# Kernel optimization log

Hardware: AMD Instinct MI355X
Metric: run time of the kernel (lower is better)

Reference implementation:

```python
import jax, jax.numpy as jnp
import numpy as np

N = 100000   # nodes
E = 1000000  # edges
G = 256      # graphs
IN, HID, OUT = 64, 64, 32


def _gcn_conv(x, W, b, src, dst, n_nodes):
    # PyG GCNConv with add_self_loops=True, symmetric normalization:
    # out = D^{-1/2} (A + I) D^{-1/2} X W + b
    h = x @ W  # [N, F]
    deg = jax.ops.segment_sum(jnp.ones_like(src, dtype=h.dtype), dst, num_segments=n_nodes) + 1.0
    dinv = jax.lax.rsqrt(deg)  # deg >= 1 due to self loops
    norm = dinv[src] * dinv[dst]  # [E]
    agg = jax.ops.segment_sum(h[src] * norm[:, None], dst, num_segments=n_nodes)
    agg = agg + h * (dinv * dinv)[:, None]  # self-loop contribution
    return agg + b


def setup_inputs() -> dict:
    key = jax.random.key(0)
    ks = jax.random.split(key, 12)
    x = jax.random.normal(ks[0], (N, IN), dtype=jnp.float32)
    edge_index = jax.random.randint(ks[1], (2, E), 0, N, dtype=jnp.int64)
    batch = jnp.sort(jax.random.randint(ks[2], (N,), 0, G, dtype=jnp.int64))

    def lin(k, fin, fout):
        s = 1.0 / np.sqrt(fin)
        kw, kb = jax.random.split(k)
        return (jax.random.uniform(kw, (fin, fout), minval=-s, maxval=s, dtype=jnp.float32),
                jax.random.uniform(kb, (fout,), minval=-s, maxval=s, dtype=jnp.float32))

    W1, b1 = lin(ks[3], IN, HID)
    W2, b2 = lin(ks[4], HID, HID)
    Wmu, bmu = lin(ks[5], HID, OUT)
    Wlv, blv = lin(ks[6], HID, OUT)
    Wd1, bd1 = lin(ks[7], OUT, HID)
    Wd2, bd2 = lin(ks[8], HID, IN)
    return {"x": x, "edge_index": edge_index, "batch": batch,
            "W1": W1, "b1": b1, "W2": W2, "b2": b2,
            "Wmu": Wmu, "bmu": bmu, "Wlv": Wlv, "blv": blv,
            "Wd1": Wd1, "bd1": bd1, "Wd2": Wd2, "bd2": bd2}


def reference(x, edge_index, batch, W1, b1, W2, b2, Wmu, bmu, Wlv, blv, Wd1, bd1, Wd2, bd2):
    src, dst = edge_index[0], edge_index[1]
    h = jax.nn.relu(_gcn_conv(x, W1, b1, src, dst, N))
    h = jax.nn.relu(_gcn_conv(h, W2, b2, src, dst, N))
    # global mean pool per graph
    sums = jax.ops.segment_sum(h, batch, num_segments=G)
    counts = jax.ops.segment_sum(jnp.ones((N,), dtype=h.dtype), batch, num_segments=G)
    pooled = sums / jnp.maximum(counts, 1.0)[:, None]  # [G, HID]
    mu = pooled @ Wmu + bmu
    logvar = pooled @ Wlv + blv
    eps = jax.random.normal(jax.random.key(42), mu.shape, dtype=mu.dtype)
    z = mu + eps * jnp.exp(0.5 * logvar)
    recon = jax.nn.relu(z @ Wd1 + bd1) @ Wd2 + bd2  # [G, IN]
    return recon, mu, logvar
```

## Files before the change

### kernel.cpp

```cpp
#include <hip/hip_runtime.h>
#include <hip/hip_bf16.h>

typedef __attribute__((ext_vector_type(8))) short bf16x8;
typedef __attribute__((ext_vector_type(4))) float f32x4;

__device__ inline unsigned short f2bf(float f) {
    unsigned u = __float_as_uint(f);
    unsigned r = u + 0x7fffu + ((u >> 16) & 1u);
    return (unsigned short)(r >> 16);
}
__device__ inline float bf2f(unsigned short s) {
    return __uint_as_float((unsigned)s << 16);
}


__device__ inline unsigned rotl32(unsigned x, unsigned r) {
    return (x << r) | (x >> (32 - r));
}

__device__ inline void threefry2x32_042(unsigned c0, unsigned c1,
                                        unsigned& o0, unsigned& o1) {
    const unsigned k0 = 0u, k1 = 42u;
    unsigned ks[3] = { k0, k1, k0 ^ k1 ^ 0x1BD11BDAu };
    unsigned x0 = c0 + ks[0];
    unsigned x1 = c1 + ks[1];
    const unsigned rotA[4] = {13u, 15u, 26u, 6u};
    const unsigned rotB[4] = {17u, 29u, 16u, 24u};

    #pragma unroll
    for (int i = 0; i < 5; ++i) {
        #pragma unroll
        for (int j = 0; j < 4; ++j) {
            unsigned r = (i & 1) ? rotB[j] : rotA[j];
            x0 += x1;
            x1 = rotl32(x1, r);
            x1 ^= x0;
        }
        x0 += ks[(i + 1) % 3];
        x1 += ks[(i + 2) % 3] + (unsigned)(i + 1);
    }
    o0 = x0; o1 = x1;
}

__device__ inline float erfinv_f32(float x) {
    float w = -log1pf(-x * x);
    float p;
    if (w < 5.0f) {
        w -= 2.5f;
        p = 2.81022636e-08f;
        p = fmaf(p, w, 3.43273939e-07f);
        p = fmaf(p, w, -3.5233877e-06f);
        p = fmaf(p, w, -4.39150654e-06f);
        p = fmaf(p, w, 0.00021858087f);
        p = fmaf(p, w, -0.00125372503f);
        p = fmaf(p, w, -0.00417768164f);
        p = fmaf(p, w, 0.246640727f);
        p = fmaf(p, w, 1.50140941f);
    } else {
        w = sqrtf(w) - 3.0f;
        p = -0.000200214257f;
        p = fmaf(p, w, 0.000100950558f);
        p = fmaf(p, w, 0.00134934322f);
        p = fmaf(p, w, -0.00367342844f);
        p = fmaf(p, w, 0.00573950773f);
        p = fmaf(p, w, -0.0076224613f);
        p = fmaf(p, w, 0.00943887047f);
        p = fmaf(p, w, 1.00167406f);
        p = fmaf(p, w, 2.83297682f);
    }
    return p * x;
}

__device__ inline float jax_normal_4232(unsigned idx) {
    unsigned o0, o1;
    threefry2x32_042(0u, idx, o0, o1);
    unsigned bits = o0 ^ o1;
    unsigned fb = (bits >> 9) | 0x3f800000u;
    float f = __uint_as_float(fb) - 1.0f;
    const float lo = -0.99999994f;
    float u = f * (1.0f - lo) + lo;
    u = fmaxf(u, lo);
    return 1.41421356f * erfinv_f32(u);
}


__device__ inline int idx_at(const void* p, long long i, int is64) {
    return is64 ? (int)((const long long*)p)[i] : ((const int*)p)[i];
}

#define NBK 256
#define CAP 4864

__global__ __launch_bounds__(256) void detect_idx64(const unsigned* __restrict__ raw,
                                                    int ne, int* flag,
                                                    int* __restrict__ bcnt,
                                                    int* __restrict__ gcur) {
    __shared__ int nz;
    if (threadIdx.x == 0) nz = 0;
    bcnt[threadIdx.x] = 0;
    gcur[threadIdx.x] = threadIdx.x * CAP;
    __syncthreads();
    int stride = ne / 2048;
    if (stride < 1) stride = 1;
    for (int k = threadIdx.x; k < 2048; k += 256) {
        long long j = (long long)k * stride;
        if (j < ne && raw[2 * j + 1] != 0u) nz = 1;
    }
    __syncthreads();
    if (threadIdx.x == 0) flag[0] = (nz == 0) ? 1 : 0;
}


#define CHUNK_MAX 4096

__global__ __launch_bounds__(256) void bucket_fill(const void* __restrict__ ei,
                                                   const int* __restrict__ flag,
                                                   int* __restrict__ gcur,
                                                   int* __restrict__ bcnt,
                                                   int2* __restrict__ pairs,
                                                   int ne, int npb, int chunk) {
    __shared__ int hist[NBK];
    __shared__ int basecur[NBK];
    __shared__ int sbuf[CHUNK_MAX];
    __shared__ int dbuf[CHUNK_MAX];
    int t = threadIdx.x;
    hist[t] = 0;
    __syncthreads();
    int is64 = flag[0];
    int c0 = blockIdx.x * chunk;
    int c1 = c0 + chunk; if (c1 > ne) c1 = ne;
    for (int i = c0 + t; i < c1; i += 256) {
        int s = idx_at(ei, i, is64);
        int d = idx_at(ei, (long long)ne + i, is64);
        sbuf[i - c0] = s;
        dbuf[i - c0] = d;
        atomicAdd(&hist[d / npb], 1);
    }
    __syncthreads();
    if (hist[t] > 0) {
        basecur[t] = atomicAdd(&gcur[t], hist[t]);
        atomicAdd(&bcnt[t], hist[t]);
    }
    __syncthreads();
    int nloc = c1 - c0;
    for (int li = t; li < nloc; li += 256) {
        int d = dbuf[li];
        int bb = d / npb;
        int slot = atomicAdd(&basecur[bb], 1);
        if (slot < (bb + 1) * CAP) pairs[slot] = make_int2(sbuf[li], d);
    }
}

#define NPB_MAX 512
__global__ __launch_bounds__(256) void csr_build(const int2* __restrict__ pairs,
                                                 const int* __restrict__ bcnt,
                                                 int* __restrict__ rowptr,
                                                 int* __restrict__ degarr,
                                                 float* __restrict__ dinv,
                                                 int* __restrict__ csr_src,
                                                 float* __restrict__ sums, int gtot,
                                                 int n, int npb) {
    __shared__ int cnt[NPB_MAX];
    __shared__ int cur[NPB_MAX];
    int b = blockIdx.x;
    int t = threadIdx.x;
    int gi = b * 256 + t;
    if (gi < gtot) sums[gi] = 0.0f;
    int bstart = b * npb;
    int bn = n - bstart; if (bn > npb) bn = npb;
    if (bn <= 0) return;
    int e0 = b * CAP;
    int count = bcnt[b]; if (count > CAP) count = CAP;
    int e1 = e0 + count;

    for (int i = t; i < bn; i += 256) cnt[i] = 0;
    __syncthreads();
    for (int i = e0 + t; i < e1; i += 256)
        atomicAdd(&cnt[pairs[i].y - bstart], 1);
    __syncthreads();

    if (t < 64) {
        int running = 0;
        for (int base2 = 0; base2 < bn; base2 += 64) {
            int idx2 = base2 + t;
            int v = (idx2 < bn) ? cnt[idx2] : 0;
            int orig = v;
            #pragma unroll
            for (int off = 1; off < 64; off <<= 1) {
                int tmp = __shfl_up(v, off);
                if (t >= off) v += tmp;
            }
            if (idx2 < bn) cur[idx2] = e0 + running + (v - orig);
            running += __shfl(v, 63);
        }
    }
    __syncthreads();

    for (int ln = t; ln < bn; ln += 256) {
        rowptr[bstart + ln] = cur[ln];
        degarr[bstart + ln] = cnt[ln];
        dinv[bstart + ln] = rsqrtf((float)cnt[ln] + 1.0f);
    }
    __syncthreads();

    for (int i = e0 + t; i < e1; i += 256) {
        int2 p = pairs[i];
        int slot = atomicAdd(&cur[p.y - bstart], 1);
        csr_src[slot] = p.x;
    }
}


__device__ inline void load_wfrags(const float* __restrict__ W,
                                   int cq, int cr, bf16x8 wf[2][4]) {
    #pragma unroll
    for (int ks = 0; ks < 2; ++ks)
        #pragma unroll
        for (int cb = 0; cb < 4; ++cb) {
            bf16x8 v;
            #pragma unroll
            for (int j = 0; j < 8; ++j) {
                int k = ks * 32 + cq * 8 + j;
                v[j] = (short)f2bf(W[k * 64 + cb * 16 + cr]);
            }
            wf[ks][cb] = v;
        }
}

__device__ inline void mfma_store(f32x4 acc[4], const float* __restrict__ dinv,
                                  unsigned short* __restrict__ Y,
                                  int rowbase, int cq, int cr, int nrows) {
    #pragma unroll
    for (int reg = 0; reg < 4; ++reg) {
        int r = rowbase + cq * 4 + reg;
        if (r < nrows) {
            float dv = dinv[r];
            #pragma unroll
            for (int cb = 0; cb < 4; ++cb)
                Y[(size_t)r * 64 + cb * 16 + cr] = f2bf(acc[cb][reg] * dv);
        }
    }
}

__global__ __launch_bounds__(256) void lin64_mfma_f32(const float* __restrict__ X,
                                                      const float* __restrict__ W,
                                                      const float* __restrict__ dinv,
                                                      unsigned short* __restrict__ Y,
                                                      int nrows) {
    int t = threadIdx.x;
    int lane = t & 63, wid = t >> 6;
    int cq = lane >> 4, cr = lane & 15;
    bf16x8 wf[2][4];
    load_wfrags(W, cq, cr, wf);
    int rowbase = (blockIdx.x * 4 + wid) * 16;
    if (rowbase >= nrows) return;
    int arow = rowbase + cr; if (arow >= nrows) arow = nrows - 1;
    const float* xr = X + (size_t)arow * 64;
    bf16x8 af[2];
    #pragma unroll
    for (int ks = 0; ks < 2; ++ks) {
        const float4* p = (const float4*)(xr + ks * 32 + cq * 8);
        float4 a = p[0], b = p[1];
        bf16x8 v;
        v[0] = (short)f2bf(a.x); v[1] = (short)f2bf(a.y);
        v[2] = (short)f2bf(a.z); v[3] = (short)f2bf(a.w);
        v[4] = (short)f2bf(b.x); v[5] = (short)f2bf(b.y);
        v[6] = (short)f2bf(b.z); v[7] = (short)f2bf(b.w);
        af[ks] = v;
    }
    f32x4 z = {0.0f, 0.0f, 0.0f, 0.0f};
    f32x4 acc[4] = {z, z, z, z};
    #pragma unroll
    for (int ks = 0; ks < 2; ++ks)
        #pragma unroll
        for (int cb = 0; cb < 4; ++cb)
            acc[cb] = __builtin_amdgcn_mfma_f32_16x16x32_bf16(af[ks], wf[ks][cb],
                                                              acc[cb], 0, 0, 0);
    mfma_store(acc, dinv, Y, rowbase, cq, cr, nrows);
}

__global__ __launch_bounds__(256) void lin64_mfma_bf16(const unsigned short* __restrict__ X,
                                                       const float* __restrict__ bin,
                                                       const float* __restrict__ W,
                                                       const float* __restrict__ dinv,
                                                       unsigned short* __restrict__ Y,
                                                       int nrows) {
    int t = threadIdx.x;
    int lane = t & 63, wid = t >> 6;
    int cq = lane >> 4, cr = lane & 15;
    bf16x8 wf[2][4];
    load_wfrags(W, cq, cr, wf);
    float bpre[2][8];
    #pragma unroll
    for (int ks = 0; ks < 2; ++ks)
        #pragma unroll
        for (int j = 0; j < 8; ++j)
            bpre[ks][j] = bin[ks * 32 + cq * 8 + j];
    int rowbase = (blockIdx.x * 4 + wid) * 16;
    if (rowbase >= nrows) return;
    int arow = rowbase + cr; if (arow >= nrows) arow = nrows - 1;
    const unsigned short* xr = X + (size_t)arow * 64;
    bf16x8 af[2];
    #pragma unroll
    for (int ks = 0; ks < 2; ++ks) {
        bf16x8 raw = *(const bf16x8*)(xr + ks * 32 + cq * 8);
        bf16x8 v;
        #pragma unroll
        for (int j = 0; j < 8; ++j) {
            float vv = bf2f((unsigned short)raw[j]) + bpre[ks][j];
            v[j] = (short)f2bf(fmaxf(vv, 0.0f));
        }
        af[ks] = v;
    }
    f32x4 z = {0.0f, 0.0f, 0.0f, 0.0f};
    f32x4 acc[4] = {z, z, z, z};
    #pragma unroll
    for (int ks = 0; ks < 2; ++ks)
        #pragma unroll
        for (int cb = 0; cb < 4; ++cb)
            acc[cb] = __builtin_amdgcn_mfma_f32_16x16x32_bf16(af[ks], wf[ks][cb],
                                                              acc[cb], 0, 0, 0);
    mfma_store(acc, dinv, Y, rowbase, cq, cr, nrows);
}


__global__ __launch_bounds__(256) void gcn_gather(const unsigned short* __restrict__ A,
                                                  const float* __restrict__ dinv,
                                                  const int* __restrict__ rowptr,
                                                  const int* __restrict__ degarr,
                                                  const int* __restrict__ csr_src,
                                                  unsigned short* __restrict__ B, int n) {
    int t = threadIdx.x;
    int node = blockIdx.x * 4 + (t >> 6);
    int c = t & 63;
    if (node >= n) return;
    float acc = bf2f(A[(size_t)node * 64 + c]);
    int beg = rowptr[node];
    int mt = degarr[node];
    for (int chunk = 0; chunk < mt; chunk += 64) {
        int m = mt - chunk; if (m > 64) m = 64;
        int sl = (c < m) ? csr_src[beg + chunk + c] : 0;
        for (int j0 = 0; j0 < m; j0 += 16) {
            int mm = m - j0; if (mm > 16) mm = 16;
            int sidx[16];
            #pragma unroll
            for (int j = 0; j < 16; ++j)
                sidx[j] = __shfl(sl, j < mm ? j0 + j : j0);
            float v[16];
            #pragma unroll
            for (int j = 0; j < 16; ++j)
                v[j] = bf2f(A[(size_t)sidx[j] * 64 + c]);
            #pragma unroll
            for (int j = 0; j < 16; ++j)
                v[j] = (j < mm) ? v[j] : 0.0f;
            float s01 = (v[0] + v[1]) + (v[2] + v[3]);
            float s23 = (v[4] + v[5]) + (v[6] + v[7]);
            float s45 = (v[8] + v[9]) + (v[10] + v[11]);
            float s67 = (v[12] + v[13]) + (v[14] + v[15]);
            acc += (s01 + s23) + (s45 + s67);
        }
    }
    B[(size_t)node * 64 + c] = f2bf(acc * dinv[node]);
}

#define POOL_NPW 32
__global__ __launch_bounds__(256) void pool_seg(const __hip_bfloat16* __restrict__ X,
                                                const float* __restrict__ b,
                                                const void* __restrict__ batch,
                                                const int* __restrict__ flag,
                                                float* __restrict__ sums,
                                                float* __restrict__ counts, int n) {
    int t = threadIdx.x;
    int c = t & 63;
    int wid = blockIdx.x * 4 + (t >> 6);
    int s0 = wid * POOL_NPW;
    if (s0 >= n) return;
    int s1 = s0 + POOL_NPW; if (s1 > n) s1 = n;
    int is64 = flag[0];
    float bc = b[c];
    float acc = 0.0f, cnt = 0.0f;
    int cur = idx_at(batch, s0, is64);
    int i = s0;
    for (; i + 2 <= s1; i += 2) {
        int g0 = idx_at(batch, i, is64);
        int g1 = idx_at(batch, i + 1, is64);
        float v0 = __bfloat162float(X[(size_t)i * 64 + c]);
        float v1 = __bfloat162float(X[(size_t)(i + 1) * 64 + c]);
        if (g0 != cur) {
            atomicAdd(&sums[(size_t)cur * 64 + c], acc);
            if (c == 0) atomicAdd(&counts[cur], cnt);
            acc = 0.0f; cnt = 0.0f; cur = g0;
        }
        acc += fmaxf(v0 + bc, 0.0f); cnt += 1.0f;
        if (g1 != cur) {
            atomicAdd(&sums[(size_t)cur * 64 + c], acc);
            if (c == 0) atomicAdd(&counts[cur], cnt);
            acc = 0.0f; cnt = 0.0f; cur = g1;
        }
        acc += fmaxf(v1 + bc, 0.0f); cnt += 1.0f;
    }
    if (i < s1) {
        int g0 = idx_at(batch, i, is64);
        float v0 = __bfloat162float(X[(size_t)i * 64 + c]);
        if (g0 != cur) {
            atomicAdd(&sums[(size_t)cur * 64 + c], acc);
            if (c == 0) atomicAdd(&counts[cur], cnt);
            acc = 0.0f; cnt = 0.0f; cur = g0;
        }
        acc += fmaxf(v0 + bc, 0.0f); cnt += 1.0f;
    }
    atomicAdd(&sums[(size_t)cur * 64 + c], acc);
    if (c == 0) atomicAdd(&counts[cur], cnt);
}

__global__ __launch_bounds__(64) void vae_head(const float* __restrict__ sums,
                                               const float* __restrict__ counts,
                                               const float* __restrict__ Wmu,
                                               const float* __restrict__ bmu,
                                               const float* __restrict__ Wlv,
                                               const float* __restrict__ blv,
                                               const float* __restrict__ Wd1,
                                               const float* __restrict__ bd1,
                                               const float* __restrict__ Wd2,
                                               const float* __restrict__ bd2,
                                               float* __restrict__ out) {
    int g = blockIdx.x;
    int t = threadIdx.x;
    __shared__ float sp[64];
    __shared__ float sz[32];
    __shared__ float sh[64];

    float cnt = fmaxf(counts[g], 1.0f);
    sp[t] = sums[(size_t)g * 64 + t] / cnt;
    __syncthreads();

    if (t < 32) {
        float mu = bmu[t];
        float lv = blv[t];
        #pragma unroll
        for (int k = 0; k < 64; ++k) {
            float pk = sp[k];
            mu = fmaf(pk, Wmu[k * 32 + t], mu);
            lv = fmaf(pk, Wlv[k * 32 + t], lv);
        }
        unsigned idx = (unsigned)(g * 32 + t);
        float eps = jax_normal_4232(idx);
        float z = fmaf(eps, expf(0.5f * lv), mu);
        sz[t] = z;
        out[16384 + (size_t)g * 32 + t] = mu;
        out[24576 + (size_t)g * 32 + t] = lv;
    }
    __syncthreads();

    float h = bd1[t];
    #pragma unroll
    for (int k = 0; k < 32; ++k) h = fmaf(sz[k], Wd1[k * 64 + t], h);
    h = fmaxf(h, 0.0f);
    sh[t] = h;
    __syncthreads();

    float r = bd2[t];
    #pragma unroll
    for (int k = 0; k < 64; ++k) r = fmaf(sh[k], Wd2[k * 64 + t], r);
    out[(size_t)g * 64 + t] = r;
}


extern "C" void kernel_launch(void* const* d_in, const int* in_sizes, int n_in,
                              void* d_out, int out_size, void* d_ws, size_t ws_size,
                              hipStream_t stream) {
    const float* x    = (const float*)d_in[0];
    const void*  ei   = d_in[1];
    const void*  batch= d_in[2];
    const float* W1   = (const float*)d_in[3];
    const float* b1   = (const float*)d_in[4];
    const float* W2   = (const float*)d_in[5];
    const float* b2   = (const float*)d_in[6];
    const float* Wmu  = (const float*)d_in[7];
    const float* bmu  = (const float*)d_in[8];
    const float* Wlv  = (const float*)d_in[9];
    const float* blv  = (const float*)d_in[10];
    const float* Wd1  = (const float*)d_in[11];
    const float* bd1  = (const float*)d_in[12];
    const float* Wd2  = (const float*)d_in[13];
    const float* bd2  = (const float*)d_in[14];

    const int N = in_sizes[0] / 64;
    const int E = in_sizes[1] / 2;
    const int G = 256;

    const int NPB = (N + NBK - 1) / NBK;
    const int nbu = (N + NPB - 1) / NPB;

    float* out = (float*)d_out;

    float* dinv = (float*)d_ws;
    __hip_bfloat16* A = (__hip_bfloat16*)(dinv + ((N + 255) & ~255));
    __hip_bfloat16* B = A + (size_t)N * 64;
    float* sums = (float*)(B + (size_t)N * 64);
    float* cnts = sums + (size_t)G * 64;
    int*   flag = (int*)(cnts + G);
    int*   rowptr = flag + 256;
    int*   degarr = rowptr + ((N + 255) & ~255);
    int*   bcnt = degarr + ((N + 255) & ~255);
    int*   gcur = bcnt + 256;
    int*   csr_src = gcur + 256;
    int2*  pairs = (int2*)(csr_src + (((size_t)nbu * CAP + 1) & ~1ull));

    const int blkRows  = (N + 3) / 4;
    const int blkLin   = (N + 63) / 64;
    const int blkPool  = (N + POOL_NPW * 4 - 1) / (POOL_NPW * 4);
    const int chunkE   = (E + NBK - 1) / NBK;
    const int gtot     = G * 64 + G;

    detect_idx64<<<1, 256, 0, stream>>>((const unsigned*)ei, E, flag, bcnt, gcur);

    bucket_fill<<<NBK, 256, 0, stream>>>(ei, flag, gcur, bcnt, pairs, E, NPB, chunkE);
    csr_build<<<nbu, 256, 0, stream>>>(pairs, bcnt, rowptr, degarr, dinv, csr_src,
                                       sums, gtot, N, NPB);

    lin64_mfma_f32<<<blkLin, 256, 0, stream>>>(x, W1, dinv, (unsigned short*)A, N);
    gcn_gather<<<blkRows, 256, 0, stream>>>((const unsigned short*)A, dinv,
                                            rowptr, degarr, csr_src,
                                            (unsigned short*)B, N);

    lin64_mfma_bf16<<<blkLin, 256, 0, stream>>>((const unsigned short*)B, b1, W2,
                                                dinv, (unsigned short*)A, N);
    gcn_gather<<<blkRows, 256, 0, stream>>>((const unsigned short*)A, dinv,
                                            rowptr, degarr, csr_src,
                                            (unsigned short*)B, N);

    pool_seg<<<blkPool, 256, 0, stream>>>(B, b2, batch, flag, sums, cnts, N);
    vae_head<<<G, 64, 0, stream>>>(sums, cnts, Wmu, bmu, Wlv, blv,
                                   Wd1, bd1, Wd2, bd2, out);
}
```

Measured before the change: 160.4 us.

## Pack edge pairs into 32-bit words, process two nodes per wave in gather

The CSR build now packs each edge's local destination and source into one 32-bit word (dest<<17 | src), with the bucket id kept in a byte buffer. This halves the pairs traffic and shared-memory staging in bucket_fill and csr_build. The gather kernel now handles two nodes per wavefront and interleaves their first 16 neighbor loads, giving each wave more memory requests in flight. pool_seg halves nodes per wave and unrolls by 4. The packing relies on node ids below 2^17 and per-bucket local indices fitting in 15 bits, which holds for N=100000.

```diff
diff --git a/kernel.cpp b/kernel.cpp
--- a/kernel.cpp
+++ b/kernel.cpp
@@ -117,12 +117,12 @@
                                                    const int* __restrict__ flag,
                                                    int* __restrict__ gcur,
                                                    int* __restrict__ bcnt,
-                                                   int2* __restrict__ pairs,
+                                                   int* __restrict__ pairs,
                                                    int ne, int npb, int chunk) {
     __shared__ int hist[NBK];
     __shared__ int basecur[NBK];
-    __shared__ int sbuf[CHUNK_MAX];
-    __shared__ int dbuf[CHUNK_MAX];
+    __shared__ int pbuf[CHUNK_MAX];
+    __shared__ unsigned char bbuf[CHUNK_MAX];
     int t = threadIdx.x;
     hist[t] = 0;
     __syncthreads();
@@ -132,9 +132,11 @@
     for (int i = c0 + t; i < c1; i += 256) {
         int s = idx_at(ei, i, is64);
         int d = idx_at(ei, (long long)ne + i, is64);
-        sbuf[i - c0] = s;
-        dbuf[i - c0] = d;
-        atomicAdd(&hist[d / npb], 1);
+        int bb = d / npb;
+        int dloc = d - bb * npb;
+        pbuf[i - c0] = (dloc << 17) | s;
+        bbuf[i - c0] = (unsigned char)bb;
+        atomicAdd(&hist[bb], 1);
     }
     __syncthreads();
     if (hist[t] > 0) {
@@ -144,15 +146,14 @@
     __syncthreads();
     int nloc = c1 - c0;
     for (int li = t; li < nloc; li += 256) {
-        int d = dbuf[li];
-        int bb = d / npb;
+        int bb = bbuf[li];
         int slot = atomicAdd(&basecur[bb], 1);
-        if (slot < (bb + 1) * CAP) pairs[slot] = make_int2(sbuf[li], d);
+        if (slot < (bb + 1) * CAP) pairs[slot] = pbuf[li];
     }
 }
 
 #define NPB_MAX 512
-__global__ __launch_bounds__(256) void csr_build(const int2* __restrict__ pairs,
+__global__ __launch_bounds__(256) void csr_build(const int* __restrict__ pairs,
                                                  const int* __restrict__ bcnt,
                                                  int* __restrict__ rowptr,
                                                  int* __restrict__ degarr,
@@ -176,7 +177,7 @@
     for (int i = t; i < bn; i += 256) cnt[i] = 0;
     __syncthreads();
     for (int i = e0 + t; i < e1; i += 256)
-        atomicAdd(&cnt[pairs[i].y - bstart], 1);
+        atomicAdd(&cnt[pairs[i] >> 17], 1);
     __syncthreads();
 
     if (t < 64) {
@@ -204,9 +205,9 @@
     __syncthreads();
 
     for (int i = e0 + t; i < e1; i += 256) {
-        int2 p = pairs[i];
-        int slot = atomicAdd(&cur[p.y - bstart], 1);
-        csr_src[slot] = p.x;
+        int p = pairs[i];
+        int slot = atomicAdd(&cur[p >> 17], 1);
+        csr_src[slot] = p & 0x1FFFF;
     }
 }
 
@@ -324,6 +325,32 @@
 }
 
 
+__device__ inline float tree16(const float v[16]) {
+    float s0 = (v[0] + v[1]) + (v[2] + v[3]);
+    float s1 = (v[4] + v[5]) + (v[6] + v[7]);
+    float s2 = (v[8] + v[9]) + (v[10] + v[11]);
+    float s3 = (v[12] + v[13]) + (v[14] + v[15]);
+    return (s0 + s1) + (s2 + s3);
+}
+
+__device__ inline float gather_rounds(const unsigned short* __restrict__ A,
+                                      int c, int sl, int f, int start) {
+    float acc = 0.0f;
+    for (int j0 = start; j0 < f; j0 += 16) {
+        int mm = f - j0; if (mm > 16) mm = 16;
+        int sidx[16];
+        #pragma unroll
+        for (int j = 0; j < 16; ++j) sidx[j] = __shfl(sl, j < mm ? j0 + j : 0);
+        float v[16];
+        #pragma unroll
+        for (int j = 0; j < 16; ++j) v[j] = bf2f(A[(size_t)sidx[j] * 64 + c]);
+        #pragma unroll
+        for (int j = 0; j < 16; ++j) v[j] = (j < mm) ? v[j] : 0.0f;
+        acc += tree16(v);
+    }
+    return acc;
+}
+
 __global__ __launch_bounds__(256) void gcn_gather(const unsigned short* __restrict__ A,
                                                   const float* __restrict__ dinv,
                                                   const int* __restrict__ rowptr,
@@ -331,39 +358,64 @@
                                                   const int* __restrict__ csr_src,
                                                   unsigned short* __restrict__ B, int n) {
     int t = threadIdx.x;
-    int node = blockIdx.x * 4 + (t >> 6);
+    int wid = t >> 6;
     int c = t & 63;
-    if (node >= n) return;
-    float acc = bf2f(A[(size_t)node * 64 + c]);
-    int beg = rowptr[node];
-    int mt = degarr[node];
-    for (int chunk = 0; chunk < mt; chunk += 64) {
-        int m = mt - chunk; if (m > 64) m = 64;
-        int sl = (c < m) ? csr_src[beg + chunk + c] : 0;
-        for (int j0 = 0; j0 < m; j0 += 16) {
-            int mm = m - j0; if (mm > 16) mm = 16;
-            int sidx[16];
-            #pragma unroll
-            for (int j = 0; j < 16; ++j)
-                sidx[j] = __shfl(sl, j < mm ? j0 + j : j0);
-            float v[16];
-            #pragma unroll
-            for (int j = 0; j < 16; ++j)
-                v[j] = bf2f(A[(size_t)sidx[j] * 64 + c]);
-            #pragma unroll
-            for (int j = 0; j < 16; ++j)
-                v[j] = (j < mm) ? v[j] : 0.0f;
-            float s01 = (v[0] + v[1]) + (v[2] + v[3]);
-            float s23 = (v[4] + v[5]) + (v[6] + v[7]);
-            float s45 = (v[8] + v[9]) + (v[10] + v[11]);
-            float s67 = (v[12] + v[13]) + (v[14] + v[15]);
-            acc += (s01 + s23) + (s45 + s67);
-        }
-    }
-    B[(size_t)node * 64 + c] = f2bf(acc * dinv[node]);
-}
-
-#define POOL_NPW 32
+    int n0 = (blockIdx.x * 4 + wid) * 2;
+    if (n0 >= n) return;
+    int has1 = (n0 + 1 < n);
+    int n1 = has1 ? n0 + 1 : n0;
+
+    float acc0 = bf2f(A[(size_t)n0 * 64 + c]);
+    float acc1 = bf2f(A[(size_t)n1 * 64 + c]);
+    int beg0 = rowptr[n0], m0 = degarr[n0];
+    int beg1 = rowptr[n1], m1 = has1 ? degarr[n1] : 0;
+
+    int f0 = m0 > 64 ? 64 : m0;
+    int f1 = m1 > 64 ? 64 : m1;
+    int sl0 = (c < f0) ? csr_src[beg0 + c] : 0;
+    int sl1 = (c < f1) ? csr_src[beg1 + c] : 0;
+
+    {
+        int mm0 = f0 > 16 ? 16 : f0;
+        int mm1 = f1 > 16 ? 16 : f1;
+        int s0i[16], s1i[16];
+        #pragma unroll
+        for (int j = 0; j < 16; ++j) {
+            s0i[j] = __shfl(sl0, j < mm0 ? j : 0);
+            s1i[j] = __shfl(sl1, j < mm1 ? j : 0);
+        }
+        float v0[16], v1[16];
+        #pragma unroll
+        for (int j = 0; j < 16; ++j) v0[j] = bf2f(A[(size_t)s0i[j] * 64 + c]);
+        #pragma unroll
+        for (int j = 0; j < 16; ++j) v1[j] = bf2f(A[(size_t)s1i[j] * 64 + c]);
+        #pragma unroll
+        for (int j = 0; j < 16; ++j) {
+            v0[j] = (j < mm0) ? v0[j] : 0.0f;
+            v1[j] = (j < mm1) ? v1[j] : 0.0f;
+        }
+        acc0 += tree16(v0);
+        acc1 += tree16(v1);
+    }
+
+    if (f0 > 16) acc0 += gather_rounds(A, c, sl0, f0, 16);
+    for (int chunk = 64; chunk < m0; chunk += 64) {
+        int rem = m0 - chunk; int f = rem > 64 ? 64 : rem;
+        int sl = (c < f) ? csr_src[beg0 + chunk + c] : 0;
+        acc0 += gather_rounds(A, c, sl, f, 0);
+    }
+    if (f1 > 16) acc1 += gather_rounds(A, c, sl1, f1, 16);
+    for (int chunk = 64; chunk < m1; chunk += 64) {
+        int rem = m1 - chunk; int f = rem > 64 ? 64 : rem;
+        int sl = (c < f) ? csr_src[beg1 + chunk + c] : 0;
+        acc1 += gather_rounds(A, c, sl, f, 0);
+    }
+
+    B[(size_t)n0 * 64 + c] = f2bf(acc0 * dinv[n0]);
+    if (has1) B[(size_t)n1 * 64 + c] = f2bf(acc1 * dinv[n1]);
+}
+
+#define POOL_NPW 16
 __global__ __launch_bounds__(256) void pool_seg(const __hip_bfloat16* __restrict__ X,
                                                 const float* __restrict__ b,
                                                 const void* __restrict__ batch,
@@ -381,11 +433,15 @@
     float acc = 0.0f, cnt = 0.0f;
     int cur = idx_at(batch, s0, is64);
     int i = s0;
-    for (; i + 2 <= s1; i += 2) {
-        int g0 = idx_at(batch, i, is64);
+    for (; i + 4 <= s1; i += 4) {
+        int g0 = idx_at(batch, i + 0, is64);
         int g1 = idx_at(batch, i + 1, is64);
-        float v0 = __bfloat162float(X[(size_t)i * 64 + c]);
+        int g2 = idx_at(batch, i + 2, is64);
+        int g3 = idx_at(batch, i + 3, is64);
+        float v0 = __bfloat162float(X[(size_t)(i + 0) * 64 + c]);
         float v1 = __bfloat162float(X[(size_t)(i + 1) * 64 + c]);
+        float v2 = __bfloat162float(X[(size_t)(i + 2) * 64 + c]);
+        float v3 = __bfloat162float(X[(size_t)(i + 3) * 64 + c]);
         if (g0 != cur) {
             atomicAdd(&sums[(size_t)cur * 64 + c], acc);
             if (c == 0) atomicAdd(&counts[cur], cnt);
@@ -398,8 +454,20 @@
             acc = 0.0f; cnt = 0.0f; cur = g1;
         }
         acc += fmaxf(v1 + bc, 0.0f); cnt += 1.0f;
-    }
-    if (i < s1) {
+        if (g2 != cur) {
+            atomicAdd(&sums[(size_t)cur * 64 + c], acc);
+            if (c == 0) atomicAdd(&counts[cur], cnt);
+            acc = 0.0f; cnt = 0.0f; cur = g2;
+        }
+        acc += fmaxf(v2 + bc, 0.0f); cnt += 1.0f;
+        if (g3 != cur) {
+            atomicAdd(&sums[(size_t)cur * 64 + c], acc);
+            if (c == 0) atomicAdd(&counts[cur], cnt);
+            acc = 0.0f; cnt = 0.0f; cur = g3;
+        }
+        acc += fmaxf(v3 + bc, 0.0f); cnt += 1.0f;
+    }
+    for (; i < s1; ++i) {
         int g0 = idx_at(batch, i, is64);
         float v0 = __bfloat162float(X[(size_t)i * 64 + c]);
         if (g0 != cur) {
@@ -505,9 +573,9 @@
     int*   bcnt = degarr + ((N + 255) & ~255);
     int*   gcur = bcnt + 256;
     int*   csr_src = gcur + 256;
-    int2*  pairs = (int2*)(csr_src + (((size_t)nbu * CAP + 1) & ~1ull));
-
-    const int blkRows  = (N + 3) / 4;
+    int*   pairs = csr_src + (size_t)nbu * CAP;
+
+    const int blkGather = (N + 7) / 8;
     const int blkLin   = (N + 63) / 64;
     const int blkPool  = (N + POOL_NPW * 4 - 1) / (POOL_NPW * 4);
     const int chunkE   = (E + NBK - 1) / NBK;
@@ -520,15 +588,15 @@
                                        sums, gtot, N, NPB);
 
     lin64_mfma_f32<<<blkLin, 256, 0, stream>>>(x, W1, dinv, (unsigned short*)A, N);
-    gcn_gather<<<blkRows, 256, 0, stream>>>((const unsigned short*)A, dinv,
-                                            rowptr, degarr, csr_src,
-                                            (unsigned short*)B, N);
+    gcn_gather<<<blkGather, 256, 0, stream>>>((const unsigned short*)A, dinv,
+                                              rowptr, degarr, csr_src,
+                                              (unsigned short*)B, N);
 
     lin64_mfma_bf16<<<blkLin, 256, 0, stream>>>((const unsigned short*)B, b1, W2,
                                                 dinv, (unsigned short*)A, N);
-    gcn_gather<<<blkRows, 256, 0, stream>>>((const unsigned short*)A, dinv,
-                                            rowptr, degarr, csr_src,
-                                            (unsigned short*)B, N);
+    gcn_gather<<<blkGather, 256, 0, stream>>>((const unsigned short*)A, dinv,
+                                              rowptr, degarr, csr_src,
+                                              (unsigned short*)B, N);
 
     pool_seg<<<blkPool, 256, 0, stream>>>(B, b2, batch, flag, sums, cnts, N);
     vae_head<<<G, 64, 0, stream>>>(sums, cnts, Wmu, bmu, Wlv, blv,
```

Result: no change. 162.2 us (+1.1%).
